# Performance work log

Hardware: AMD Instinct MI355X
Metric: run time of the kernel (lower is better)

## Reference

```python
import jax, jax.numpy as jnp
import numpy as np

B, S, D, H = 2, 2048, 512, 8
HS = D // H  # head_size = 64


def setup_inputs() -> dict:
    key = jax.random.key(0)
    ks = jax.random.split(key, 6)
    scale = 1.0 / np.sqrt(D)
    return {
        "seq_input": jax.random.normal(ks[0], (B, S, D), dtype=jnp.float32),
        "w_X": jax.random.uniform(ks[1], (B, S, S), dtype=jnp.float32),
        "mask": jax.random.uniform(ks[2], (B, S), dtype=jnp.float32),
        "wq": jax.random.normal(ks[3], (D, D), dtype=jnp.float32) * scale,
        "bq": jnp.zeros((D,), dtype=jnp.float32),
        "wk": jax.random.normal(ks[4], (D, D), dtype=jnp.float32) * scale,
        "bk": jnp.zeros((D,), dtype=jnp.float32),
        "wv": jax.random.normal(ks[5], (D, D), dtype=jnp.float32) * scale,
        "bv": jnp.zeros((D,), dtype=jnp.float32),
    }


def reference(seq_input, w_X, mask, wq, bq, wk, bk, wv, bv):
    b, s, d = seq_input.shape
    # Linear projections, split into heads: [b, h, s, hs]
    def proj(w, bias):
        y = jnp.einsum("bsd,ed->bse", seq_input, w) + bias
        return y.reshape(b, s, H, HS).transpose(0, 2, 1, 3)

    Q = proj(wq, bq)
    K = proj(wk, bk)
    V = proj(wv, bv)

    sim = jnp.einsum("bhqe,bhke->bhqk", Q, K) / np.sqrt(HS).astype(np.float32)
    sim = jax.nn.softmax(sim, axis=3)
    # post-softmax multiplicative edge weights, broadcast over heads
    sim = sim * w_X[:, None, :, :]
    # mask zeroes query rows (torch permute trick broadcasts mask over key dim)
    sim = sim * mask[:, None, :, None]

    new_V = jnp.einsum("bhqk,bhke->bhqe", sim, V)  # [b, h, s, hs]
    return new_V.transpose(0, 2, 1, 3).reshape(b, s, d)
```

## Files before the change

### kernel.cpp

```cpp
#include <hip/hip_runtime.h>

typedef __attribute__((ext_vector_type(4))) float f32x4;
typedef __attribute__((ext_vector_type(8))) short s16x8;
typedef __attribute__((ext_vector_type(2))) unsigned int u32x2;

__device__ inline unsigned short f2bf(float f) {
  unsigned int u = __float_as_uint(f);
  unsigned int r = (u + 0x7FFFu + ((u >> 16) & 1u)) >> 16;
  return (unsigned short)r;
}
__device__ inline int swz(int row, int col) { return row * 64 + (col ^ ((row & 7) << 3)); }

__device__ inline s16x8 pack8(const f32x4& a0, const f32x4& a1) {
  s16x8 v;
#pragma unroll
  for (int j = 0; j < 4; ++j) { v[j] = (short)f2bf(a0[j]); v[4 + j] = (short)f2bf(a1[j]); }
  return v;
}

__global__ __launch_bounds__(512) void kv_kernel(
    const float* __restrict__ X, const float* __restrict__ wk, const float* __restrict__ wv,
    const float* __restrict__ bk, const float* __restrict__ bv,
    unsigned short* __restrict__ Kb, unsigned short* __restrict__ Vt) {
  __shared__ __align__(16) unsigned short As[64 * 64];
  __shared__ __align__(16) unsigned short Bs[128 * 64];
  const int tid = threadIdx.x;
  const int lane = tid & 63, wid = tid >> 6;
  const int lr = lane & 15, lh = lane >> 4;
  const int m0 = blockIdx.y * 64;
  const int nb = blockIdx.x;
  const int type = nb >> 2;
  const int wrow0 = (nb & 3) * 128;
  const float* W = (type == 0) ? wk : wv;
  const float* bias = (type == 0) ? bk : bv;
  const int wm = wid >> 2, wn = wid & 3;

  f32x4 acc[2][2] = {};
  f32x4 ar[2], br[2][2];

#define KV_LOAD(K0)                                                          \
  {                                                                          \
    { int row = tid >> 3, c8 = (tid & 7) * 8;                                \
      const float* pa = X + (size_t)(m0 + row) * 512 + (K0) + c8;            \
      ar[0] = *(const f32x4*)pa; ar[1] = *(const f32x4*)(pa + 4); }          \
    _Pragma("unroll") for (int g = 0; g < 2; ++g) {                          \
      int idx = tid + 512 * g; int row = idx >> 3, c8 = (idx & 7) * 8;       \
      const float* pb = W + (size_t)(wrow0 + row) * 512 + (K0) + c8;         \
      br[g][0] = *(const f32x4*)pb; br[g][1] = *(const f32x4*)(pb + 4);      \
    }                                                                        \
  }

  KV_LOAD(0);
  for (int k0 = 0; k0 < 512; k0 += 64) {
    {
      int row = tid >> 3, c8 = (tid & 7) * 8;
      *(s16x8*)&As[swz(row, c8)] = pack8(ar[0], ar[1]);
    }
#pragma unroll
    for (int g = 0; g < 2; ++g) {
      int idx = tid + 512 * g; int row = idx >> 3, c8 = (idx & 7) * 8;
      *(s16x8*)&Bs[swz(row, c8)] = pack8(br[g][0], br[g][1]);
    }
    __syncthreads();
    if (k0 < 448) KV_LOAD(k0 + 64);
#pragma unroll
    for (int kk = 0; kk < 64; kk += 32) {
      s16x8 af[2], bf_[2];
#pragma unroll
      for (int f = 0; f < 2; ++f) af[f] = *(const s16x8*)&As[swz(wm * 32 + f * 16 + lr, kk + lh * 8)];
#pragma unroll
      for (int f = 0; f < 2; ++f) bf_[f] = *(const s16x8*)&Bs[swz(wn * 32 + f * 16 + lr, kk + lh * 8)];
#pragma unroll
      for (int fm = 0; fm < 2; ++fm)
#pragma unroll
        for (int fn = 0; fn < 2; ++fn)
          acc[fm][fn] = __builtin_amdgcn_mfma_f32_16x16x32_bf16(af[fm], bf_[fn], acc[fm][fn], 0, 0, 0);
    }
    __syncthreads();
  }
#undef KV_LOAD

#pragma unroll
  for (int fn = 0; fn < 2; ++fn) {
    int n = wrow0 + wn * 32 + fn * 16 + lr;
    int hh = n >> 6, hs = n & 63;
    float bb = bias[n];
#pragma unroll
    for (int fm = 0; fm < 2; ++fm) {
#pragma unroll
      for (int r = 0; r < 4; ++r) {
        int m = m0 + wm * 32 + fm * 16 + lh * 4 + r;
        int b = m >> 11, s = m & 2047;
        float val = acc[fm][fn][r] + bb;
        if (type == 0) {
          Kb[((size_t)(b * 8 + hh) * 2048 + s) * 64 + hs] = f2bf(val);
        } else {
          Vt[((size_t)(b * 8 + hh) * 64 + hs) * 2048 + s] = f2bf(val);
        }
      }
    }
  }
}

__global__ __launch_bounds__(256) void attn_kernel(
    const float* __restrict__ X, const float* __restrict__ wq, const float* __restrict__ bq,
    const unsigned short* __restrict__ Kb, const unsigned short* __restrict__ Vt,
    const float* __restrict__ wX, const float* __restrict__ mask, float* __restrict__ out) {
  __shared__ __align__(16) unsigned short Ks[64 * 64];
  __shared__ __align__(16) unsigned short Vs[64 * 64];
  __shared__ __align__(16) unsigned short Qs[64 * 64];
  __shared__ __align__(16) unsigned short Ps[4 * 16 * 64];
  const int tid = threadIdx.x;
  const int lane = tid & 63, wid = tid >> 6;
  const int lr = lane & 15, lh = lane >> 4;
  const int qt = blockIdx.x, hh = blockIdx.y, b = blockIdx.z;
  const int bh = b * 8 + hh;
  const int q0 = qt * 64;

  const int srow = tid >> 3, sc8 = (tid & 7) * 8;
  const int srow1 = (tid + 256) >> 3;

  f32x4 qacc[4] = {};
  f32x4 xr[2][2], wr0[2][2];
#define Q_LOAD(K0)                                                           \
  {                                                                          \
    _Pragma("unroll") for (int g = 0; g < 2; ++g) {                          \
      int row = g ? srow1 : srow;                                            \
      const float* px = X + (size_t)(b * 2048 + q0 + row) * 512 + (K0) + sc8;\
      const float* pw = wq + (size_t)(hh * 64 + row) * 512 + (K0) + sc8;     \
      xr[g][0] = *(const f32x4*)px; xr[g][1] = *(const f32x4*)(px + 4);      \
      wr0[g][0] = *(const f32x4*)pw; wr0[g][1] = *(const f32x4*)(pw + 4);    \
    }                                                                        \
  }
  Q_LOAD(0);
  for (int k0 = 0; k0 < 512; k0 += 64) {
#pragma unroll
    for (int g = 0; g < 2; ++g) {
      int row = g ? srow1 : srow;
      *(s16x8*)&Ks[swz(row, sc8)] = pack8(xr[g][0], xr[g][1]);
      *(s16x8*)&Vs[swz(row, sc8)] = pack8(wr0[g][0], wr0[g][1]);
    }
    __syncthreads();
    if (k0 < 448) Q_LOAD(k0 + 64);
#pragma unroll
    for (int kk = 0; kk < 64; kk += 32) {
      s16x8 xa = *(const s16x8*)&Ks[swz(wid * 16 + lr, kk + lh * 8)];
#pragma unroll
      for (int fn = 0; fn < 4; ++fn) {
        s16x8 wf = *(const s16x8*)&Vs[swz(fn * 16 + lr, kk + lh * 8)];
        qacc[fn] = __builtin_amdgcn_mfma_f32_16x16x32_bf16(xa, wf, qacc[fn], 0, 0, 0);
      }
    }
    __syncthreads();
  }
#undef Q_LOAD

  const int qrow_base = q0 + wid * 16 + lh * 4;
  const int q_sm = q0 + wid * 16 + lr;
  const float* wxq = wX + ((size_t)b * 2048 + q_sm) * 2048;

  s16x8 kreg[2], vreg[2];
  f32x4 wxv[4];
#define KV_TILE_LOAD(KT)                                                     \
  {                                                                          \
    _Pragma("unroll") for (int g = 0; g < 2; ++g) {                          \
      int row = g ? srow1 : srow;                                            \
      kreg[g] = *(const s16x8*)(Kb + ((size_t)bh * 2048 + (KT) * 64 + row) * 64 + sc8); \
      vreg[g] = *(const s16x8*)(Vt + ((size_t)bh * 64 + row) * 2048 + (KT) * 64 + sc8); \
    }                                                                        \
  }
#define WX_LOAD(KT)                                                          \
  {                                                                          \
    _Pragma("unroll") for (int f = 0; f < 4; ++f)                            \
      wxv[f] = *(const f32x4*)(wxq + (KT) * 64 + f * 16 + lh * 4);           \
  }
  KV_TILE_LOAD(0);
  WX_LOAD(0);

#pragma unroll
  for (int fn = 0; fn < 4; ++fn) {
    int col = fn * 16 + lr;
    float bb = bq[hh * 64 + col];
#pragma unroll
    for (int r = 0; r < 4; ++r) {
      int row = wid * 16 + lh * 4 + r;
      Qs[swz(row, col)] = f2bf((qacc[fn][r] + bb) * 0.125f);
    }
  }
  __syncthreads();

  s16x8 qa[2];
#pragma unroll
  for (int c = 0; c < 2; ++c) qa[c] = *(const s16x8*)&Qs[swz(wid * 16 + lr, c * 32 + lh * 8)];

  float m_ = -__builtin_inff(), l_ = 0.f;
  f32x4 o[4] = {};

  for (int kt = 0; kt < 32; ++kt) {
#pragma unroll
    for (int g = 0; g < 2; ++g) {
      int row = g ? srow1 : srow;
      *(s16x8*)&Ks[swz(row, sc8)] = kreg[g];
      *(s16x8*)&Vs[swz(row, sc8)] = vreg[g];
    }
    __syncthreads();
    if (kt + 1 < 32) KV_TILE_LOAD(kt + 1);

    f32x4 sv[4] = {};
#pragma unroll
    for (int c = 0; c < 2; ++c) {
#pragma unroll
      for (int f = 0; f < 4; ++f) {
        s16x8 kf = *(const s16x8*)&Ks[swz(f * 16 + lr, c * 32 + lh * 8)];
        sv[f] = __builtin_amdgcn_mfma_f32_16x16x32_bf16(kf, qa[c], sv[f], 0, 0, 0);
      }
    }

    float t0 = fmaxf(fmaxf(sv[0][0], sv[0][1]), fmaxf(sv[0][2], sv[0][3]));
    float t1 = fmaxf(fmaxf(sv[1][0], sv[1][1]), fmaxf(sv[1][2], sv[1][3]));
    float t2 = fmaxf(fmaxf(sv[2][0], sv[2][1]), fmaxf(sv[2][2], sv[2][3]));
    float t3 = fmaxf(fmaxf(sv[3][0], sv[3][1]), fmaxf(sv[3][2], sv[3][3]));
    float tm = fmaxf(fmaxf(t0, t1), fmaxf(t2, t3));
    tm = fmaxf(tm, __shfl_xor(tm, 16));
    tm = fmaxf(tm, __shfl_xor(tm, 32));

    float nm = fmaxf(m_, tm);
    float sc = __expf(m_ - nm);
    m_ = nm;
    l_ *= sc;
    float sc_o[4];
#pragma unroll
    for (int r = 0; r < 4; ++r) sc_o[r] = __shfl(sc, 20 * lh + r);
#pragma unroll
    for (int f = 0; f < 4; ++f)
#pragma unroll
      for (int r = 0; r < 4; ++r) o[f][r] *= sc_o[r];

    float ls = 0.f;
#pragma unroll
    for (int f = 0; f < 4; ++f) {
      float pw[4];
#pragma unroll
      for (int r = 0; r < 4; ++r) {
        float p = __expf(sv[f][r] - m_);
        ls += p;
        pw[r] = p * wxv[f][r];
      }
      u32x2 pk;
      pk[0] = (unsigned int)f2bf(pw[0]) | ((unsigned int)f2bf(pw[1]) << 16);
      pk[1] = (unsigned int)f2bf(pw[2]) | ((unsigned int)f2bf(pw[3]) << 16);
      *(u32x2*)&Ps[wid * 1024 + swz(lr, f * 16 + lh * 4)] = pk;
    }
    if (kt + 1 < 32) WX_LOAD(kt + 1);
    ls += __shfl_xor(ls, 16);
    ls += __shfl_xor(ls, 32);
    l_ += ls;

#pragma unroll
    for (int c = 0; c < 2; ++c) {
      s16x8 pf = *(const s16x8*)&Ps[wid * 1024 + swz(lr, c * 32 + lh * 8)];
#pragma unroll
      for (int f = 0; f < 4; ++f) {
        s16x8 vf = *(const s16x8*)&Vs[swz(f * 16 + lr, c * 32 + lh * 8)];
        o[f] = __builtin_amdgcn_mfma_f32_16x16x32_bf16(pf, vf, o[f], 0, 0, 0);
      }
    }
    __syncthreads();
  }
#undef KV_TILE_LOAD
#undef WX_LOAD

  float l_o[4];
#pragma unroll
  for (int r = 0; r < 4; ++r) l_o[r] = __shfl(l_, 20 * lh + r);
#pragma unroll
  for (int r = 0; r < 4; ++r) {
    int q = qrow_base + r;
    float mk = mask[b * 2048 + q];
    float inv = mk / l_o[r];
#pragma unroll
    for (int f = 0; f < 4; ++f) {
      out[((size_t)(b * 2048 + q)) * 512 + hh * 64 + f * 16 + lr] = o[f][r] * inv;
    }
  }
}

extern "C" void kernel_launch(void* const* d_in, const int* in_sizes, int n_in,
                              void* d_out, int out_size, void* d_ws, size_t ws_size,
                              hipStream_t stream) {
  const float* X = (const float*)d_in[0];
  const float* wX = (const float*)d_in[1];
  const float* mask = (const float*)d_in[2];
  const float* wq = (const float*)d_in[3];
  const float* bq = (const float*)d_in[4];
  const float* wk = (const float*)d_in[5];
  const float* bk = (const float*)d_in[6];
  const float* wv = (const float*)d_in[7];
  const float* bv = (const float*)d_in[8];
  float* out = (float*)d_out;

  unsigned short* Kb = (unsigned short*)d_ws;
  unsigned short* Vt = Kb + 2097152;

  kv_kernel<<<dim3(8, 64), 512, 0, stream>>>(X, wk, wv, bk, bv, Kb, Vt);
  attn_kernel<<<dim3(32, 8, 2), 256, 0, stream>>>(X, wq, bq, Kb, Vt, wX, mask, out);
}
```

Baseline: 164.7 us.

## Double-buffer K/V and Q-projection shared tiles to drop one barrier per iteration

Shared K and V tiles become two buffers, both in the Q-projection loop and in the attention loop. The next tile is written into the alternate buffer while the current one is consumed, and global prefetch now runs two tiles ahead. This removes one __syncthreads per iteration and overlaps LDS stores with MFMA work. The cost is twice the LDS for K and V, which may lower occupancy, plus more live registers.

```diff
diff --git a/kernel.cpp b/kernel.cpp
--- a/kernel.cpp
+++ b/kernel.cpp
@@ -106,8 +106,8 @@
     const float* __restrict__ X, const float* __restrict__ wq, const float* __restrict__ bq,
     const unsigned short* __restrict__ Kb, const unsigned short* __restrict__ Vt,
     const float* __restrict__ wX, const float* __restrict__ mask, float* __restrict__ out) {
-  __shared__ __align__(16) unsigned short Ks[64 * 64];
-  __shared__ __align__(16) unsigned short Vs[64 * 64];
+  __shared__ __align__(16) unsigned short Ks[2][64 * 64];
+  __shared__ __align__(16) unsigned short Vs[2][64 * 64];
   __shared__ __align__(16) unsigned short Qs[64 * 64];
   __shared__ __align__(16) unsigned short Ps[4 * 16 * 64];
   const int tid = threadIdx.x;
@@ -133,25 +133,25 @@
     }                                                                        \
   }
   Q_LOAD(0);
-  for (int k0 = 0; k0 < 512; k0 += 64) {
+  for (int s = 0; s < 8; ++s) {
+    const int cur = s & 1;
 #pragma unroll
     for (int g = 0; g < 2; ++g) {
       int row = g ? srow1 : srow;
-      *(s16x8*)&Ks[swz(row, sc8)] = pack8(xr[g][0], xr[g][1]);
-      *(s16x8*)&Vs[swz(row, sc8)] = pack8(wr0[g][0], wr0[g][1]);
-    }
+      *(s16x8*)&Ks[cur][swz(row, sc8)] = pack8(xr[g][0], xr[g][1]);
+      *(s16x8*)&Vs[cur][swz(row, sc8)] = pack8(wr0[g][0], wr0[g][1]);
+    }
+    if (s < 7) Q_LOAD((s + 1) * 64);
     __syncthreads();
-    if (k0 < 448) Q_LOAD(k0 + 64);
 #pragma unroll
     for (int kk = 0; kk < 64; kk += 32) {
-      s16x8 xa = *(const s16x8*)&Ks[swz(wid * 16 + lr, kk + lh * 8)];
+      s16x8 xa = *(const s16x8*)&Ks[cur][swz(wid * 16 + lr, kk + lh * 8)];
 #pragma unroll
       for (int fn = 0; fn < 4; ++fn) {
-        s16x8 wf = *(const s16x8*)&Vs[swz(fn * 16 + lr, kk + lh * 8)];
+        s16x8 wf = *(const s16x8*)&Vs[cur][swz(fn * 16 + lr, kk + lh * 8)];
         qacc[fn] = __builtin_amdgcn_mfma_f32_16x16x32_bf16(xa, wf, qacc[fn], 0, 0, 0);
       }
     }
-    __syncthreads();
   }
 #undef Q_LOAD
 
@@ -189,29 +189,39 @@
   }
   __syncthreads();
 
+#pragma unroll
+  for (int g = 0; g < 2; ++g) {
+    int row = g ? srow1 : srow;
+    *(s16x8*)&Ks[0][swz(row, sc8)] = kreg[g];
+    *(s16x8*)&Vs[0][swz(row, sc8)] = vreg[g];
+  }
   s16x8 qa[2];
 #pragma unroll
   for (int c = 0; c < 2; ++c) qa[c] = *(const s16x8*)&Qs[swz(wid * 16 + lr, c * 32 + lh * 8)];
+  KV_TILE_LOAD(1);
+  __syncthreads();
 
   float m_ = -__builtin_inff(), l_ = 0.f;
   f32x4 o[4] = {};
 
   for (int kt = 0; kt < 32; ++kt) {
-#pragma unroll
-    for (int g = 0; g < 2; ++g) {
-      int row = g ? srow1 : srow;
-      *(s16x8*)&Ks[swz(row, sc8)] = kreg[g];
-      *(s16x8*)&Vs[swz(row, sc8)] = vreg[g];
-    }
-    __syncthreads();
-    if (kt + 1 < 32) KV_TILE_LOAD(kt + 1);
+    const int cur = kt & 1;
+    if (kt < 31) {
+#pragma unroll
+      for (int g = 0; g < 2; ++g) {
+        int row = g ? srow1 : srow;
+        *(s16x8*)&Ks[cur ^ 1][swz(row, sc8)] = kreg[g];
+        *(s16x8*)&Vs[cur ^ 1][swz(row, sc8)] = vreg[g];
+      }
+    }
+    if (kt < 30) KV_TILE_LOAD(kt + 2);
 
     f32x4 sv[4] = {};
 #pragma unroll
     for (int c = 0; c < 2; ++c) {
 #pragma unroll
       for (int f = 0; f < 4; ++f) {
-        s16x8 kf = *(const s16x8*)&Ks[swz(f * 16 + lr, c * 32 + lh * 8)];
+        s16x8 kf = *(const s16x8*)&Ks[cur][swz(f * 16 + lr, c * 32 + lh * 8)];
         sv[f] = __builtin_amdgcn_mfma_f32_16x16x32_bf16(kf, qa[c], sv[f], 0, 0, 0);
       }
     }
@@ -261,7 +271,7 @@
       s16x8 pf = *(const s16x8*)&Ps[wid * 1024 + swz(lr, c * 32 + lh * 8)];
 #pragma unroll
       for (int f = 0; f < 4; ++f) {
-        s16x8 vf = *(const s16x8*)&Vs[swz(f * 16 + lr, c * 32 + lh * 8)];
+        s16x8 vf = *(const s16x8*)&Vs[cur][swz(f * 16 + lr, c * 32 + lh * 8)];
         o[f] = __builtin_amdgcn_mfma_f32_16x16x32_bf16(pf, vf, o[f], 0, 0, 0);
       }
     }
```

Measured after the change: 177.2 us. +7.6%, slower.
